# Kernel optimization log

Hardware: AMD Instinct MI355X
Metric: run time of the kernel (lower is better)

## Reference

```python
import jax, jax.numpy as jnp
import numpy as np

N, M = 50000, 32
HID, FILT, NBR = 128, 128, 64


def setup_inputs() -> dict:
    key = jax.random.key(0)
    ks = jax.random.split(key, 12)
    s = lambda fan_in: 1.0 / np.sqrt(fan_in)
    return {
        "node_repr": jax.random.normal(ks[0], (N, HID), dtype=jnp.float32),
        "nbr_fea": jax.random.normal(ks[1], (N, M, NBR), dtype=jnp.float32),
        "nbr_fea_idx": jax.random.randint(ks[2], (N, M), 0, N, dtype=jnp.int64),
        # filter_net: Linear(NBR, FILT) -> SiLU -> Linear(FILT, HID)
        "fw1": jax.random.uniform(ks[3], (NBR, FILT), jnp.float32, -s(NBR), s(NBR)),
        "fb1": jax.random.uniform(ks[4], (FILT,), jnp.float32, -s(NBR), s(NBR)),
        "fw2": jax.random.uniform(ks[5], (FILT, HID), jnp.float32, -s(FILT), s(FILT)),
        "fb2": jax.random.uniform(ks[6], (HID,), jnp.float32, -s(FILT), s(FILT)),
        # update: Linear(HID, HID) -> SiLU -> Linear(HID, HID)
        "uw1": jax.random.uniform(ks[7], (HID, HID), jnp.float32, -s(HID), s(HID)),
        "ub1": jax.random.uniform(ks[8], (HID,), jnp.float32, -s(HID), s(HID)),
        "uw2": jax.random.uniform(ks[9], (HID, HID), jnp.float32, -s(HID), s(HID)),
        "ub2": jax.random.uniform(ks[10], (HID,), jnp.float32, -s(HID), s(HID)),
    }


def reference(node_repr, nbr_fea, nbr_fea_idx, fw1, fb1, fw2, fb2, uw1, ub1, uw2, ub2):
    # gather neighbor representations: [N, M, HID]
    neighbor_repr = node_repr[nbr_fea_idx]
    # continuous filters from neighbor features: [N, M, HID]
    h = jax.nn.silu(jnp.einsum("nmf,fk->nmk", nbr_fea, fw1) + fb1)
    filters = jnp.einsum("nmk,kh->nmh", h, fw2) + fb2
    # filter-weighted sum over neighbors: [N, HID]
    message = jnp.sum(neighbor_repr * filters, axis=1)
    # update MLP
    u = jax.nn.silu(message @ uw1 + ub1)
    return u @ uw2 + ub2
```

## Files before the change

kernel.cpp:

```cpp
#include <hip/hip_runtime.h>


#define NN 50000
#define MM 32
#define HID 128
#define NBR 64

typedef __attribute__((ext_vector_type(4))) float f32x4;
typedef __attribute__((ext_vector_type(8))) short s16x8;
typedef __attribute__((ext_vector_type(4))) short s16x4;

__device__ __forceinline__ short f2bf(float x) {
  unsigned u = __builtin_bit_cast(unsigned, x);
  unsigned r = (u + 0x7FFFu + ((u >> 16) & 1u)) >> 16;
  return (short)r;
}

__device__ __forceinline__ float bf2f(short b) {
  return __builtin_bit_cast(float, (unsigned)(unsigned short)b << 16);
}

__device__ __forceinline__ float silu(float x) {
  return x / (1.0f + __expf(-x));
}

__global__ __launch_bounds__(256) void k_cvt_node(
    const float* __restrict__ in, short* __restrict__ out)
{
  int i = blockIdx.x * 256 + threadIdx.x;
  if (i < NN * HID / 4) {
    f32x4 v = *(reinterpret_cast<const f32x4*>(in) + i);
    s16x4 o;
    #pragma unroll
    for (int r = 0; r < 4; ++r) o[r] = f2bf(v[r]);
    reinterpret_cast<s16x4*>(out)[i] = o;
  }
}

__global__ __launch_bounds__(256, 2) void k_filter_message(
    const short* __restrict__ node_bf, const float* __restrict__ nbr_fea,
    const int* __restrict__ nbr_idx, const float* __restrict__ fw1,
    const float* __restrict__ fb1, const float* __restrict__ fw2,
    const float* __restrict__ fb2, float* __restrict__ msg_out)
{
  __shared__ __align__(16) short s_w1[128 * 72];
  __shared__ __align__(16) short s_w2[128 * 136];
  __shared__ float s_b1[128];
  __shared__ __align__(16) float s_b2[128];
  __shared__ __align__(16) short s_ft[4][16 * 136];

  const int tid = threadIdx.x;
  for (int i = tid; i < 64 * 128; i += 256) {
    int k = i >> 7, f = i & 127;
    s_w1[f * 72 + k] = f2bf(fw1[i]);
  }
  for (int i = tid; i < 128 * 128; i += 256) {
    int k = i >> 7, h = i & 127;
    s_w2[h * 136 + k] = f2bf(fw2[i]);
  }
  if (tid < 128) { s_b1[tid] = fb1[tid]; s_b2[tid] = fb2[tid]; }
  __syncthreads();

  const int wave = tid >> 6, lane = tid & 63;
  const int c = lane & 15, g = lane >> 4;
  const int r = lane >> 3, k = lane & 7;
  short* __restrict__ ft = s_ft[wave];
  const int gw = blockIdx.x * 4 + wave;
  const int STRIDE = 512 * 4;

  int vidx[2][2];
  #pragma unroll
  for (int mt = 0; mt < 2; ++mt)
    #pragma unroll
    for (int i = 0; i < 2; ++i)
      vidx[mt][i] = nbr_idx[(size_t)gw * MM + mt * 16 + 8 * i + r];

  for (int n = gw; n < NN; n += STRIDE) {
    s16x8 gr[2][2][2];
    #pragma unroll
    for (int mt = 0; mt < 2; ++mt)
      #pragma unroll
      for (int i = 0; i < 2; ++i) {
        const short* rp = node_bf + (size_t)vidx[mt][i] * HID + 8 * k;
        gr[mt][i][0] = *reinterpret_cast<const s16x8*>(rp);
        gr[mt][i][1] = *reinterpret_cast<const s16x8*>(rp + 64);
      }

    const float* nf = nbr_fea + (size_t)n * (MM * NBR);
    s16x8 b1[2][2];
    #pragma unroll
    for (int mt = 0; mt < 2; ++mt)
      #pragma unroll
      for (int kt = 0; kt < 2; ++kt) {
        const f32x4* src = reinterpret_cast<const f32x4*>(
            nf + (mt * 16 + c) * NBR + kt * 32 + g * 8);
        f32x4 lo = __builtin_nontemporal_load(src);
        f32x4 hi = __builtin_nontemporal_load(src + 1);
        s16x8 v;
        v[0] = f2bf(lo[0]); v[1] = f2bf(lo[1]); v[2] = f2bf(lo[2]); v[3] = f2bf(lo[3]);
        v[4] = f2bf(hi[0]); v[5] = f2bf(hi[1]); v[6] = f2bf(hi[2]); v[7] = f2bf(hi[3]);
        b1[mt][kt] = v;
      }

    {
      int n2 = n + STRIDE;
      int np = (n2 < NN) ? n2 : n;
      #pragma unroll
      for (int mt = 0; mt < 2; ++mt)
        #pragma unroll
        for (int i = 0; i < 2; ++i)
          vidx[mt][i] = nbr_idx[(size_t)np * MM + mt * 16 + 8 * i + r];
    }

    s16x4 P[8][2];
    #pragma unroll
    for (int t = 0; t < 8; ++t) {
      f32x4 a0 = f32x4{0.f, 0.f, 0.f, 0.f};
      f32x4 a1 = f32x4{0.f, 0.f, 0.f, 0.f};
      #pragma unroll
      for (int kt = 0; kt < 2; ++kt) {
        s16x8 w1f = *reinterpret_cast<const s16x8*>(&s_w1[(t * 16 + c) * 72 + kt * 32 + g * 8]);
        a0 = __builtin_amdgcn_mfma_f32_16x16x32_bf16(w1f, b1[0][kt], a0, 0, 0, 0);
        a1 = __builtin_amdgcn_mfma_f32_16x16x32_bf16(w1f, b1[1][kt], a1, 0, 0, 0);
      }
      s16x4 p0, p1;
      #pragma unroll
      for (int q = 0; q < 4; ++q) {
        float bias = s_b1[t * 16 + g * 4 + q];
        p0[q] = f2bf(silu(a0[q] + bias));
        p1[q] = f2bf(silu(a1[q] + bias));
      }
      P[t][0] = p0;
      P[t][1] = p1;
    }

    float part0[8], part1[8];
    #pragma unroll
    for (int j = 0; j < 8; ++j) { part0[j] = 0.f; part1[j] = 0.f; }

    #pragma unroll
    for (int mt = 0; mt < 2; ++mt) {
      #pragma unroll
      for (int ct = 0; ct < 8; ++ct) {
        f32x4 t = f32x4{0.f, 0.f, 0.f, 0.f};
        #pragma unroll
        for (int kt = 0; kt < 8; ++kt) {
          s16x4 w2f = *reinterpret_cast<const s16x4*>(&s_w2[(ct * 16 + c) * 136 + kt * 16 + g * 4]);
          t = __builtin_amdgcn_mfma_f32_16x16x16bf16_1k(w2f, P[kt][mt], t, 0, 0, 0);
        }
        f32x4 fb = *reinterpret_cast<const f32x4*>(&s_b2[ct * 16 + 4 * g]);
        s16x4 pk;
        #pragma unroll
        for (int q = 0; q < 4; ++q) pk[q] = f2bf(t[q] + fb[q]);
        *reinterpret_cast<s16x4*>(&ft[c * 136 + ct * 16 + 4 * g]) = pk;
      }
      #pragma unroll
      for (int i = 0; i < 2; ++i) {
        s16x8 f0 = *reinterpret_cast<const s16x8*>(&ft[(8 * i + r) * 136 + 8 * k]);
        s16x8 f1 = *reinterpret_cast<const s16x8*>(&ft[(8 * i + r) * 136 + 64 + 8 * k]);
        #pragma unroll
        for (int j = 0; j < 8; ++j) {
          part0[j] += bf2f(f0[j]) * bf2f(gr[mt][i][0][j]);
          part1[j] += bf2f(f1[j]) * bf2f(gr[mt][i][1][j]);
        }
      }
    }

    #pragma unroll
    for (int j = 0; j < 8; ++j) {
      part0[j] += __shfl_xor(part0[j], 8);
      part0[j] += __shfl_xor(part0[j], 16);
      part0[j] += __shfl_xor(part0[j], 32);
      part1[j] += __shfl_xor(part1[j], 8);
      part1[j] += __shfl_xor(part1[j], 16);
      part1[j] += __shfl_xor(part1[j], 32);
    }
    if (r == 0) {
      float* mp = msg_out + (size_t)n * HID + 8 * k;
      *reinterpret_cast<f32x4*>(mp)      = f32x4{part0[0], part0[1], part0[2], part0[3]};
      *reinterpret_cast<f32x4*>(mp + 4)  = f32x4{part0[4], part0[5], part0[6], part0[7]};
      *reinterpret_cast<f32x4*>(mp + 64) = f32x4{part1[0], part1[1], part1[2], part1[3]};
      *reinterpret_cast<f32x4*>(mp + 68) = f32x4{part1[4], part1[5], part1[6], part1[7]};
    }
  }
}

__global__ __launch_bounds__(256, 2) void k_update1(
    const float* __restrict__ msg, const float* __restrict__ uw1,
    const float* __restrict__ ub1, short* __restrict__ u_out)
{
  __shared__ __align__(16) short s_w1[128 * 136];
  __shared__ float s_b1[128];
  const int tid = threadIdx.x;
  for (int i = tid; i < 128 * 128; i += 256) {
    int k = i >> 7, f = i & 127;
    s_w1[f * 136 + k] = f2bf(uw1[i]);
  }
  if (tid < 128) s_b1[tid] = ub1[tid];
  __syncthreads();

  const int wave = tid >> 6, lane = tid & 63;
  const int c = lane & 15, g = lane >> 4;
  const long base = (long)(blockIdx.x * 4 + wave) * 32;
  if (base >= NN) return;

  s16x8 bfr[2][4];
  #pragma unroll
  for (int mt = 0; mt < 2; ++mt)
    #pragma unroll
    for (int kt = 0; kt < 4; ++kt) {
      long row = base + mt * 16 + c; if (row > NN - 1) row = NN - 1;
      const float* src = msg + row * HID + kt * 32 + g * 8;
      float4 lo = *reinterpret_cast<const float4*>(src);
      float4 hi = *reinterpret_cast<const float4*>(src + 4);
      s16x8 v;
      v[0] = f2bf(lo.x); v[1] = f2bf(lo.y); v[2] = f2bf(lo.z); v[3] = f2bf(lo.w);
      v[4] = f2bf(hi.x); v[5] = f2bf(hi.y); v[6] = f2bf(hi.z); v[7] = f2bf(hi.w);
      bfr[mt][kt] = v;
    }

  f32x4 acc[8][2];
  #pragma unroll
  for (int t = 0; t < 8; ++t)
    #pragma unroll
    for (int mt = 0; mt < 2; ++mt)
      acc[t][mt] = f32x4{0.f, 0.f, 0.f, 0.f};
  #pragma unroll
  for (int kt = 0; kt < 4; ++kt)
    #pragma unroll
    for (int t = 0; t < 8; ++t) {
      s16x8 a = *reinterpret_cast<const s16x8*>(&s_w1[(t * 16 + c) * 136 + kt * 32 + g * 8]);
      #pragma unroll
      for (int mt = 0; mt < 2; ++mt)
        acc[t][mt] = __builtin_amdgcn_mfma_f32_16x16x32_bf16(a, bfr[mt][kt], acc[t][mt], 0, 0, 0);
    }

  #pragma unroll
  for (int t = 0; t < 8; ++t)
    #pragma unroll
    for (int mt = 0; mt < 2; ++mt) {
      long row = base + mt * 16 + c;
      if (row < NN) {
        s16x4 p;
        #pragma unroll
        for (int q = 0; q < 4; ++q) {
          float x = acc[t][mt][q] + s_b1[t * 16 + g * 4 + q];
          p[q] = f2bf(silu(x));
        }
        *reinterpret_cast<s16x4*>(&u_out[row * HID + t * 16 + g * 4]) = p;
      }
    }
}

__global__ __launch_bounds__(256, 2) void k_update2(
    const short* __restrict__ u, const float* __restrict__ uw2,
    const float* __restrict__ ub2, float* __restrict__ out)
{
  __shared__ __align__(16) short s_w2[128 * 136];
  __shared__ float s_b2[128];
  const int tid = threadIdx.x;
  for (int i = tid; i < 128 * 128; i += 256) {
    int k = i >> 7, h = i & 127;
    s_w2[h * 136 + k] = f2bf(uw2[i]);
  }
  if (tid < 128) s_b2[tid] = ub2[tid];
  __syncthreads();

  const int wave = tid >> 6, lane = tid & 63;
  const int c = lane & 15, g = lane >> 4;
  const long base = (long)(blockIdx.x * 4 + wave) * 32;
  if (base >= NN) return;

  s16x4 afr[2][8];
  #pragma unroll
  for (int mt = 0; mt < 2; ++mt)
    #pragma unroll
    for (int kt = 0; kt < 8; ++kt) {
      long row = base + mt * 16 + c; if (row > NN - 1) row = NN - 1;
      afr[mt][kt] = *reinterpret_cast<const s16x4*>(&u[row * HID + kt * 16 + g * 4]);
    }

  f32x4 acc[8][2];
  #pragma unroll
  for (int ct = 0; ct < 8; ++ct)
    #pragma unroll
    for (int mt = 0; mt < 2; ++mt)
      acc[ct][mt] = f32x4{0.f, 0.f, 0.f, 0.f};
  #pragma unroll
  for (int ct = 0; ct < 8; ++ct)
    #pragma unroll
    for (int kt = 0; kt < 8; ++kt) {
      s16x4 b2 = *reinterpret_cast<const s16x4*>(&s_w2[(ct * 16 + c) * 136 + kt * 16 + g * 4]);
      #pragma unroll
      for (int mt = 0; mt < 2; ++mt)
        acc[ct][mt] = __builtin_amdgcn_mfma_f32_16x16x16bf16_1k(afr[mt][kt], b2, acc[ct][mt], 0, 0, 0);
    }

  #pragma unroll
  for (int ct = 0; ct < 8; ++ct) {
    const float bias = s_b2[ct * 16 + c];
    #pragma unroll
    for (int mt = 0; mt < 2; ++mt)
      #pragma unroll
      for (int q = 0; q < 4; ++q) {
        long row = base + mt * 16 + g * 4 + q;
        if (row < NN) out[row * HID + ct * 16 + c] = acc[ct][mt][q] + bias;
      }
  }
}

extern "C" void kernel_launch(void* const* d_in, const int* in_sizes, int n_in,
                              void* d_out, int out_size, void* d_ws, size_t ws_size,
                              hipStream_t stream) {
  const float* node_repr = (const float*)d_in[0];
  const float* nbr_fea   = (const float*)d_in[1];
  const int*   nbr_idx   = (const int*)d_in[2];
  const float* fw1 = (const float*)d_in[3];
  const float* fb1 = (const float*)d_in[4];
  const float* fw2 = (const float*)d_in[5];
  const float* fb2 = (const float*)d_in[6];
  const float* uw1 = (const float*)d_in[7];
  const float* ub1 = (const float*)d_in[8];
  const float* uw2 = (const float*)d_in[9];
  const float* ub2 = (const float*)d_in[10];
  float* outp = (float*)d_out;
  short* ws16 = (short*)d_ws;

  k_cvt_node<<<(NN * HID / 4 + 255) / 256, 256, 0, stream>>>(node_repr, ws16);
  k_filter_message<<<512, 256, 0, stream>>>(ws16, nbr_fea, nbr_idx,
                                            fw1, fb1, fw2, fb2, outp);
  const int rowblocks = (NN + 31) / 32;
  const int grid2 = (rowblocks + 3) / 4;
  k_update1<<<grid2, 256, 0, stream>>>(outp, uw1, ub1, ws16);
  k_update2<<<grid2, 256, 0, stream>>>(ws16, uw2, ub2, outp);
}
```

Measured before the change: 466.5 us.

## Move filter weights out of LDS to global bf16, raise occupancy and grid

Adds a small pre-kernel that converts and transposes the filter weights to bf16 in workspace. The main kernel then reads them from global/L2 instead of staging them in LDS, which cuts per-block LDS use so occupancy can rise to 4 blocks per CU, and the grid is doubled. It also stores the filters in fp32 in LDS rather than rounding to bf16, splits the neighbour gather so the second half is issued after the first GEMM, and writes the message through LDS so the global store is coalesced. The risks are more global/L2 traffic for weight fragments and extra register pressure under the tighter launch bound.

```diff
diff --git a/kernel.cpp b/kernel.cpp
--- a/kernel.cpp
+++ b/kernel.cpp
@@ -7,6 +7,7 @@
 #define NBR 64
 
 typedef __attribute__((ext_vector_type(4))) float f32x4;
+typedef __attribute__((ext_vector_type(2))) float f32x2;
 typedef __attribute__((ext_vector_type(8))) short s16x8;
 typedef __attribute__((ext_vector_type(4))) short s16x4;
 
@@ -37,36 +38,42 @@
   }
 }
 
-__global__ __launch_bounds__(256, 2) void k_filter_message(
+__global__ __launch_bounds__(256) void k_cvt_w(
+    const float* __restrict__ fw1, const float* __restrict__ fw2,
+    short* __restrict__ w1T, short* __restrict__ w2T)
+{
+  int tid = blockIdx.x * 256 + threadIdx.x;
+  int stride = gridDim.x * 256;
+  for (int i = tid; i < 64 * 128; i += stride) {
+    int k = i >> 7, f = i & 127;
+    w1T[f * 64 + k] = f2bf(fw1[i]);
+  }
+  for (int i = tid; i < 128 * 128; i += stride) {
+    int k = i >> 7, h = i & 127;
+    w2T[h * 128 + k] = f2bf(fw2[i]);
+  }
+}
+
+__global__ __launch_bounds__(256, 4) void k_filter_message(
     const short* __restrict__ node_bf, const float* __restrict__ nbr_fea,
-    const int* __restrict__ nbr_idx, const float* __restrict__ fw1,
-    const float* __restrict__ fb1, const float* __restrict__ fw2,
+    const int* __restrict__ nbr_idx, const short* __restrict__ w1T,
+    const short* __restrict__ w2T, const float* __restrict__ fb1,
     const float* __restrict__ fb2, float* __restrict__ msg_out)
 {
-  __shared__ __align__(16) short s_w1[128 * 72];
-  __shared__ __align__(16) short s_w2[128 * 136];
   __shared__ float s_b1[128];
   __shared__ __align__(16) float s_b2[128];
-  __shared__ __align__(16) short s_ft[4][16 * 136];
+  __shared__ __align__(16) float s_ft[4][16 * 132];
 
   const int tid = threadIdx.x;
-  for (int i = tid; i < 64 * 128; i += 256) {
-    int k = i >> 7, f = i & 127;
-    s_w1[f * 72 + k] = f2bf(fw1[i]);
-  }
-  for (int i = tid; i < 128 * 128; i += 256) {
-    int k = i >> 7, h = i & 127;
-    s_w2[h * 136 + k] = f2bf(fw2[i]);
-  }
   if (tid < 128) { s_b1[tid] = fb1[tid]; s_b2[tid] = fb2[tid]; }
   __syncthreads();
 
   const int wave = tid >> 6, lane = tid & 63;
   const int c = lane & 15, g = lane >> 4;
   const int r = lane >> 3, k = lane & 7;
-  short* __restrict__ ft = s_ft[wave];
+  float* __restrict__ ft = s_ft[wave];
   const int gw = blockIdx.x * 4 + wave;
-  const int STRIDE = 512 * 4;
+  const int STRIDE = 1024 * 4;
 
   int vidx[2][2];
   #pragma unroll
@@ -76,15 +83,13 @@
       vidx[mt][i] = nbr_idx[(size_t)gw * MM + mt * 16 + 8 * i + r];
 
   for (int n = gw; n < NN; n += STRIDE) {
-    s16x8 gr[2][2][2];
-    #pragma unroll
-    for (int mt = 0; mt < 2; ++mt)
-      #pragma unroll
-      for (int i = 0; i < 2; ++i) {
-        const short* rp = node_bf + (size_t)vidx[mt][i] * HID + 8 * k;
-        gr[mt][i][0] = *reinterpret_cast<const s16x8*>(rp);
-        gr[mt][i][1] = *reinterpret_cast<const s16x8*>(rp + 64);
-      }
+    s16x8 gr0[2][2];
+    #pragma unroll
+    for (int i = 0; i < 2; ++i) {
+      const short* rp = node_bf + (size_t)vidx[0][i] * HID + 8 * k;
+      gr0[i][0] = *reinterpret_cast<const s16x8*>(rp);
+      gr0[i][1] = *reinterpret_cast<const s16x8*>(rp + 64);
+    }
 
     const float* nf = nbr_fea + (size_t)n * (MM * NBR);
     s16x8 b1[2][2];
@@ -102,16 +107,6 @@
         b1[mt][kt] = v;
       }
 
-    {
-      int n2 = n + STRIDE;
-      int np = (n2 < NN) ? n2 : n;
-      #pragma unroll
-      for (int mt = 0; mt < 2; ++mt)
-        #pragma unroll
-        for (int i = 0; i < 2; ++i)
-          vidx[mt][i] = nbr_idx[(size_t)np * MM + mt * 16 + 8 * i + r];
-    }
-
     s16x4 P[8][2];
     #pragma unroll
     for (int t = 0; t < 8; ++t) {
@@ -119,7 +114,8 @@
       f32x4 a1 = f32x4{0.f, 0.f, 0.f, 0.f};
       #pragma unroll
       for (int kt = 0; kt < 2; ++kt) {
-        s16x8 w1f = *reinterpret_cast<const s16x8*>(&s_w1[(t * 16 + c) * 72 + kt * 32 + g * 8]);
+        s16x8 w1f = *reinterpret_cast<const s16x8*>(
+            w1T + (t * 16 + c) * 64 + kt * 32 + g * 8);
         a0 = __builtin_amdgcn_mfma_f32_16x16x32_bf16(w1f, b1[0][kt], a0, 0, 0, 0);
         a1 = __builtin_amdgcn_mfma_f32_16x16x32_bf16(w1f, b1[1][kt], a1, 0, 0, 0);
       }
@@ -134,6 +130,24 @@
       P[t][1] = p1;
     }
 
+    s16x8 gr1[2][2];
+    #pragma unroll
+    for (int i = 0; i < 2; ++i) {
+      const short* rp = node_bf + (size_t)vidx[1][i] * HID + 8 * k;
+      gr1[i][0] = *reinterpret_cast<const s16x8*>(rp);
+      gr1[i][1] = *reinterpret_cast<const s16x8*>(rp + 64);
+    }
+
+    {
+      int n2 = n + STRIDE;
+      int np = (n2 < NN) ? n2 : n;
+      #pragma unroll
+      for (int mt = 0; mt < 2; ++mt)
+        #pragma unroll
+        for (int i = 0; i < 2; ++i)
+          vidx[mt][i] = nbr_idx[(size_t)np * MM + mt * 16 + 8 * i + r];
+    }
+
     float part0[8], part1[8];
     #pragma unroll
     for (int j = 0; j < 8; ++j) { part0[j] = 0.f; part1[j] = 0.f; }
@@ -145,23 +159,30 @@
         f32x4 t = f32x4{0.f, 0.f, 0.f, 0.f};
         #pragma unroll
         for (int kt = 0; kt < 8; ++kt) {
-          s16x4 w2f = *reinterpret_cast<const s16x4*>(&s_w2[(ct * 16 + c) * 136 + kt * 16 + g * 4]);
+          s16x4 w2f = *reinterpret_cast<const s16x4*>(
+              w2T + (ct * 16 + c) * 128 + kt * 16 + g * 4);
           t = __builtin_amdgcn_mfma_f32_16x16x16bf16_1k(w2f, P[kt][mt], t, 0, 0, 0);
         }
         f32x4 fb = *reinterpret_cast<const f32x4*>(&s_b2[ct * 16 + 4 * g]);
-        s16x4 pk;
-        #pragma unroll
-        for (int q = 0; q < 4; ++q) pk[q] = f2bf(t[q] + fb[q]);
-        *reinterpret_cast<s16x4*>(&ft[c * 136 + ct * 16 + 4 * g]) = pk;
+        f32x4 o;
+        #pragma unroll
+        for (int q = 0; q < 4; ++q) o[q] = t[q] + fb[q];
+        *reinterpret_cast<f32x4*>(&ft[c * 132 + ct * 16 + 4 * g]) = o;
       }
       #pragma unroll
       for (int i = 0; i < 2; ++i) {
-        s16x8 f0 = *reinterpret_cast<const s16x8*>(&ft[(8 * i + r) * 136 + 8 * k]);
-        s16x8 f1 = *reinterpret_cast<const s16x8*>(&ft[(8 * i + r) * 136 + 64 + 8 * k]);
-        #pragma unroll
-        for (int j = 0; j < 8; ++j) {
-          part0[j] += bf2f(f0[j]) * bf2f(gr[mt][i][0][j]);
-          part1[j] += bf2f(f1[j]) * bf2f(gr[mt][i][1][j]);
+        const s16x8 ga = (mt == 0) ? gr0[i][0] : gr1[i][0];
+        const s16x8 gb = (mt == 0) ? gr0[i][1] : gr1[i][1];
+        f32x4 fa0 = *reinterpret_cast<const f32x4*>(&ft[(8 * i + r) * 132 + 8 * k]);
+        f32x4 fa1 = *reinterpret_cast<const f32x4*>(&ft[(8 * i + r) * 132 + 8 * k + 4]);
+        f32x4 fb0 = *reinterpret_cast<const f32x4*>(&ft[(8 * i + r) * 132 + 64 + 8 * k]);
+        f32x4 fb1 = *reinterpret_cast<const f32x4*>(&ft[(8 * i + r) * 132 + 64 + 8 * k + 4]);
+        #pragma unroll
+        for (int j = 0; j < 4; ++j) {
+          part0[j]     += fa0[j] * bf2f(ga[j]);
+          part0[j + 4] += fa1[j] * bf2f(ga[j + 4]);
+          part1[j]     += fb0[j] * bf2f(gb[j]);
+          part1[j + 4] += fb1[j] * bf2f(gb[j + 4]);
         }
       }
     }
@@ -175,13 +196,15 @@
       part1[j] += __shfl_xor(part1[j], 16);
       part1[j] += __shfl_xor(part1[j], 32);
     }
+
     if (r == 0) {
-      float* mp = msg_out + (size_t)n * HID + 8 * k;
-      *reinterpret_cast<f32x4*>(mp)      = f32x4{part0[0], part0[1], part0[2], part0[3]};
-      *reinterpret_cast<f32x4*>(mp + 4)  = f32x4{part0[4], part0[5], part0[6], part0[7]};
-      *reinterpret_cast<f32x4*>(mp + 64) = f32x4{part1[0], part1[1], part1[2], part1[3]};
-      *reinterpret_cast<f32x4*>(mp + 68) = f32x4{part1[4], part1[5], part1[6], part1[7]};
-    }
+      *reinterpret_cast<f32x4*>(&ft[8 * k])          = f32x4{part0[0], part0[1], part0[2], part0[3]};
+      *reinterpret_cast<f32x4*>(&ft[8 * k + 4])      = f32x4{part0[4], part0[5], part0[6], part0[7]};
+      *reinterpret_cast<f32x4*>(&ft[64 + 8 * k])     = f32x4{part1[0], part1[1], part1[2], part1[3]};
+      *reinterpret_cast<f32x4*>(&ft[64 + 8 * k + 4]) = f32x4{part1[4], part1[5], part1[6], part1[7]};
+    }
+    f32x2 mv = *reinterpret_cast<const f32x2*>(&ft[2 * lane]);
+    *reinterpret_cast<f32x2*>(msg_out + (size_t)n * HID + 2 * lane) = mv;
   }
 }
 
@@ -325,10 +348,13 @@
   const float* ub2 = (const float*)d_in[10];
   float* outp = (float*)d_out;
   short* ws16 = (short*)d_ws;
+  short* w1T = ws16 + (size_t)NN * HID;
+  short* w2T = w1T + 64 * 128;
 
   k_cvt_node<<<(NN * HID / 4 + 255) / 256, 256, 0, stream>>>(node_repr, ws16);
-  k_filter_message<<<512, 256, 0, stream>>>(ws16, nbr_fea, nbr_idx,
-                                            fw1, fb1, fw2, fb2, outp);
+  k_cvt_w<<<32, 256, 0, stream>>>(fw1, fw2, w1T, w2T);
+  k_filter_message<<<1024, 256, 0, stream>>>(ws16, nbr_fea, nbr_idx,
+                                             w1T, w2T, fb1, fb2, outp);
   const int rowblocks = (NN + 31) / 32;
   const int grid2 = (rowblocks + 3) / 4;
   k_update1<<<grid2, 256, 0, stream>>>(outp, uw1, ub1, ws16);
```

New measurement: 1.320 ms. 183% more time.

## Move W1 out of LDS to raise filter kernel occupancy and stage output stores

Applied to the files above, without the earlier changes.

A small pre-kernel converts fw1 to a transposed bf16 buffer in workspace. The filter kernel then reads W1 fragments from global memory, through cache, instead of keeping them in LDS. The W2 LDS row pitch shrinks from 136 to 132. The saved LDS allows 3 blocks per CU, so the grid and stride grow to 768 blocks. Message rows are also staged through the per-wave LDS buffer so all 64 lanes write coalesced float2 stores instead of 8 lanes writing. The risks are extra global-load latency on the W1 reads and possible LDS bank conflicts from the new 132 pitch.

```diff
diff --git a/kernel.cpp b/kernel.cpp
--- a/kernel.cpp
+++ b/kernel.cpp
@@ -7,6 +7,7 @@
 #define NBR 64
 
 typedef __attribute__((ext_vector_type(4))) float f32x4;
+typedef __attribute__((ext_vector_type(2))) float f32x2;
 typedef __attribute__((ext_vector_type(8))) short s16x8;
 typedef __attribute__((ext_vector_type(4))) short s16x4;
 
@@ -37,26 +38,31 @@
   }
 }
 
-__global__ __launch_bounds__(256, 2) void k_filter_message(
+__global__ __launch_bounds__(256) void k_cvt_w(
+    const float* __restrict__ fw1, short* __restrict__ w1T)
+{
+  int tid = blockIdx.x * 256 + threadIdx.x;
+  if (tid < 64 * 128) {
+    int k = tid >> 7, f = tid & 127;
+    w1T[f * 64 + k] = f2bf(fw1[tid]);
+  }
+}
+
+__global__ __launch_bounds__(256, 3) void k_filter_message(
     const short* __restrict__ node_bf, const float* __restrict__ nbr_fea,
-    const int* __restrict__ nbr_idx, const float* __restrict__ fw1,
-    const float* __restrict__ fb1, const float* __restrict__ fw2,
+    const int* __restrict__ nbr_idx, const short* __restrict__ w1T,
+    const float* __restrict__ fw2, const float* __restrict__ fb1,
     const float* __restrict__ fb2, float* __restrict__ msg_out)
 {
-  __shared__ __align__(16) short s_w1[128 * 72];
-  __shared__ __align__(16) short s_w2[128 * 136];
+  __shared__ __align__(16) short s_w2[128 * 132];
   __shared__ float s_b1[128];
   __shared__ __align__(16) float s_b2[128];
   __shared__ __align__(16) short s_ft[4][16 * 136];
 
   const int tid = threadIdx.x;
-  for (int i = tid; i < 64 * 128; i += 256) {
-    int k = i >> 7, f = i & 127;
-    s_w1[f * 72 + k] = f2bf(fw1[i]);
-  }
   for (int i = tid; i < 128 * 128; i += 256) {
     int k = i >> 7, h = i & 127;
-    s_w2[h * 136 + k] = f2bf(fw2[i]);
+    s_w2[h * 132 + k] = f2bf(fw2[i]);
   }
   if (tid < 128) { s_b1[tid] = fb1[tid]; s_b2[tid] = fb2[tid]; }
   __syncthreads();
@@ -66,7 +72,7 @@
   const int r = lane >> 3, k = lane & 7;
   short* __restrict__ ft = s_ft[wave];
   const int gw = blockIdx.x * 4 + wave;
-  const int STRIDE = 512 * 4;
+  const int STRIDE = 768 * 4;
 
   int vidx[2][2];
   #pragma unroll
@@ -119,7 +125,8 @@
       f32x4 a1 = f32x4{0.f, 0.f, 0.f, 0.f};
       #pragma unroll
       for (int kt = 0; kt < 2; ++kt) {
-        s16x8 w1f = *reinterpret_cast<const s16x8*>(&s_w1[(t * 16 + c) * 72 + kt * 32 + g * 8]);
+        s16x8 w1f = *reinterpret_cast<const s16x8*>(
+            w1T + (t * 16 + c) * 64 + kt * 32 + g * 8);
         a0 = __builtin_amdgcn_mfma_f32_16x16x32_bf16(w1f, b1[0][kt], a0, 0, 0, 0);
         a1 = __builtin_amdgcn_mfma_f32_16x16x32_bf16(w1f, b1[1][kt], a1, 0, 0, 0);
       }
@@ -145,7 +152,8 @@
         f32x4 t = f32x4{0.f, 0.f, 0.f, 0.f};
         #pragma unroll
         for (int kt = 0; kt < 8; ++kt) {
-          s16x4 w2f = *reinterpret_cast<const s16x4*>(&s_w2[(ct * 16 + c) * 136 + kt * 16 + g * 4]);
+          s16x4 w2f = *reinterpret_cast<const s16x4*>(
+              &s_w2[(ct * 16 + c) * 132 + kt * 16 + g * 4]);
           t = __builtin_amdgcn_mfma_f32_16x16x16bf16_1k(w2f, P[kt][mt], t, 0, 0, 0);
         }
         f32x4 fb = *reinterpret_cast<const f32x4*>(&s_b2[ct * 16 + 4 * g]);
@@ -175,12 +183,17 @@
       part1[j] += __shfl_xor(part1[j], 16);
       part1[j] += __shfl_xor(part1[j], 32);
     }
-    if (r == 0) {
-      float* mp = msg_out + (size_t)n * HID + 8 * k;
-      *reinterpret_cast<f32x4*>(mp)      = f32x4{part0[0], part0[1], part0[2], part0[3]};
-      *reinterpret_cast<f32x4*>(mp + 4)  = f32x4{part0[4], part0[5], part0[6], part0[7]};
-      *reinterpret_cast<f32x4*>(mp + 64) = f32x4{part1[0], part1[1], part1[2], part1[3]};
-      *reinterpret_cast<f32x4*>(mp + 68) = f32x4{part1[4], part1[5], part1[6], part1[7]};
+
+    {
+      float* fb32 = reinterpret_cast<float*>(ft);
+      if (r == 0) {
+        *reinterpret_cast<f32x4*>(&fb32[8 * k])          = f32x4{part0[0], part0[1], part0[2], part0[3]};
+        *reinterpret_cast<f32x4*>(&fb32[8 * k + 4])      = f32x4{part0[4], part0[5], part0[6], part0[7]};
+        *reinterpret_cast<f32x4*>(&fb32[64 + 8 * k])     = f32x4{part1[0], part1[1], part1[2], part1[3]};
+        *reinterpret_cast<f32x4*>(&fb32[64 + 8 * k + 4]) = f32x4{part1[4], part1[5], part1[6], part1[7]};
+      }
+      f32x2 mv = *reinterpret_cast<const f32x2*>(&fb32[2 * lane]);
+      *reinterpret_cast<f32x2*>(msg_out + (size_t)n * HID + 2 * lane) = mv;
     }
   }
 }
@@ -325,10 +338,12 @@
   const float* ub2 = (const float*)d_in[10];
   float* outp = (float*)d_out;
   short* ws16 = (short*)d_ws;
+  short* w1T = ws16 + (size_t)NN * HID;
 
   k_cvt_node<<<(NN * HID / 4 + 255) / 256, 256, 0, stream>>>(node_repr, ws16);
-  k_filter_message<<<512, 256, 0, stream>>>(ws16, nbr_fea, nbr_idx,
-                                            fw1, fb1, fw2, fb2, outp);
+  k_cvt_w<<<32, 256, 0, stream>>>(fw1, w1T);
+  k_filter_message<<<768, 256, 0, stream>>>(ws16, nbr_fea, nbr_idx,
+                                            w1T, fw2, fb1, fb2, outp);
   const int rowblocks = (NN + 31) / 32;
   const int grid2 = (rowblocks + 3) / 4;
   k_update1<<<grid2, 256, 0, stream>>>(outp, uw1, ub1, ws16);
```

Measured after the change: 1.086 ms. 133% more time.
